# Performance work log

Hardware: AMD Instinct MI355X
Metric: run time of the kernel (lower is better)

The kernel has to match this reference:

```python
import jax, jax.numpy as jnp
import numpy as np

N_NODES = 50000
N_EDGES = 800000
D_IN = 64
D_OUT = 64


def setup_inputs() -> dict:
    key = jax.random.key(0)
    k1, k2, k3, k4 = jax.random.split(key, 4)
    x = jax.random.normal(k1, (N_NODES, D_IN), dtype=jnp.float32)
    src = jax.random.randint(k2, (N_EDGES,), 0, N_NODES, dtype=jnp.int64)
    dst = jax.random.randint(k3, (N_EDGES,), 0, N_NODES, dtype=jnp.int64)
    W = jax.random.normal(k4, (D_IN, D_OUT), dtype=jnp.float32) / np.sqrt(D_IN)
    b = jnp.zeros((D_OUT,), dtype=jnp.float32)
    return {"x": x, "src": src, "dst": dst, "W": W, "b": b}


def reference(x, src, dst, W, b):
    # DGL GraphConv, norm='both': out = D_in^{-1/2} A D_out^{-1/2} x W + b
    n = x.shape[0]
    ones = jnp.ones(src.shape[0], dtype=x.dtype)
    out_deg = jax.ops.segment_sum(ones, src, num_segments=n)  # out-degree of each node
    in_deg = jax.ops.segment_sum(ones, dst, num_segments=n)   # in-degree of each node
    norm_src = jax.lax.rsqrt(jnp.clip(out_deg, 1.0))          # [N]
    norm_dst = jax.lax.rsqrt(jnp.clip(in_deg, 1.0))           # [N]
    h = x * norm_src[:, None]                                 # [N, D_in]
    msg = jnp.take(h, src, axis=0)                            # [E, D_in] gather
    agg = jax.ops.segment_sum(msg, dst, num_segments=n)       # [N, D_in] scatter-add
    agg = agg * norm_dst[:, None]
    return agg @ W + b                                        # [N, D_out]
```

## Files before the change

kernel.cpp:

```cpp
#include <hip/hip_runtime.h>

#define N_NODES 50000
#define N_EDGES 800000
#define D 64

#define SLICES 64
#define I4_PER_SLICE (N_EDGES / 4 / SLICES)
#define NWORDS 12512

#define CTR_OFF    0
#define BASE_OFF   64
#define CUR_OFF    200064
#define SNORM_OFF  400064
#define DNORM_OFF  600064
#define SSRC_OFF   800064
#define PART_OFF   4000064
#define ZERO_BYTES 64

__global__ __launch_bounds__(256) void degree_lds_kernel(const int4* __restrict__ src4,
                                                         const int4* __restrict__ dst4,
                                                         unsigned int* __restrict__ partial) {
    __shared__ unsigned int hist[NWORDS];
    int tid = threadIdx.x;
    for (int i = tid; i < NWORDS; i += 256) hist[i] = 0;
    __syncthreads();

    int role  = blockIdx.x & 1;
    int slice = blockIdx.x >> 1;
    const int4* e = role ? dst4 : src4;
    int beg = slice * I4_PER_SLICE, end = beg + I4_PER_SLICE;
    for (int i = beg + tid; i < end; i += 256) {
        int4 v = e[i];
        atomicAdd(&hist[v.x >> 2], 1u << ((v.x & 3) * 8));
        atomicAdd(&hist[v.y >> 2], 1u << ((v.y & 3) * 8));
        atomicAdd(&hist[v.z >> 2], 1u << ((v.z & 3) * 8));
        atomicAdd(&hist[v.w >> 2], 1u << ((v.w & 3) * 8));
    }
    __syncthreads();

    unsigned int* p = partial + (size_t)blockIdx.x * NWORDS;
    for (int i = tid; i < NWORDS; i += 256) p[i] = hist[i];
}

__global__ __launch_bounds__(256) void merge_scan_kernel(const unsigned int* __restrict__ partial,
                                                         int* __restrict__ base,
                                                         int* __restrict__ cursor,
                                                         float* __restrict__ snorm,
                                                         float* __restrict__ dnorm,
                                                         int* __restrict__ ctr) {
    int n = blockIdx.x * blockDim.x + threadIdx.x;
    int lane = threadIdx.x & 63;
    int din = 0, dout = 0;
    if (n < N_NODES) {
        int w = n >> 2, sh = (n & 3) * 8;
        const unsigned int* po = partial + w;
#pragma unroll 8
        for (int s = 0; s < SLICES; s++) {
            dout += (po[(size_t)(2 * s) * NWORDS] >> sh) & 0xFFu;
            din  += (po[(size_t)(2 * s + 1) * NWORDS] >> sh) & 0xFFu;
        }
    }
    int sum = din;
#pragma unroll
    for (int off = 1; off < 64; off <<= 1) {
        int v = __shfl_up(sum, off);
        if (lane >= off) sum += v;
    }
    int wtot = __shfl(sum, 63);
    int wbase = 0;
    if (lane == 63) wbase = atomicAdd(ctr, wtot);
    wbase = __shfl(wbase, 63);
    if (n < N_NODES) {
        int myb = wbase + (sum - din);
        base[n] = myb;
        cursor[n] = myb;
        dnorm[n] = rsqrtf(fmaxf((float)din, 1.0f));
        snorm[n] = rsqrtf(fmaxf((float)dout, 1.0f));
    }
}

__global__ __launch_bounds__(256) void fill_kernel(const int4* __restrict__ src4,
                                                   const int4* __restrict__ dst4,
                                                   int* __restrict__ cursor,
                                                   int* __restrict__ ssrc) {
    int i = blockIdx.x * blockDim.x + threadIdx.x;
    if (i < N_EDGES / 4) {
        int4 s = src4[i], t = dst4[i];
        int p0 = atomicAdd(&cursor[t.x], 1);
        int p1 = atomicAdd(&cursor[t.y], 1);
        int p2 = atomicAdd(&cursor[t.z], 1);
        int p3 = atomicAdd(&cursor[t.w], 1);
        ssrc[p0] = s.x; ssrc[p1] = s.y; ssrc[p2] = s.z; ssrc[p3] = s.w;
    }
}

#define GBLK 1024
__global__ __launch_bounds__(256, 4) void gather_mm_kernel(const float* __restrict__ x,
                                                           const int* __restrict__ ssrc,
                                                           const int* __restrict__ base,
                                                           const int* __restrict__ cursor,
                                                           const float* __restrict__ snorm,
                                                           const float* __restrict__ dnorm,
                                                           const float* __restrict__ W,
                                                           const float* __restrict__ b,
                                                           float* __restrict__ out) {
    int lane = threadIdx.x & 63;
    int wave = (blockIdx.x << 2) | (threadIdx.x >> 6);

    float Wreg[D];
#pragma unroll
    for (int k = 0; k < D; k++) Wreg[k] = W[k * D + lane];
    float breg = b[lane];
    const float* xl = x + lane;

    for (int n = wave; n < N_NODES; n += GBLK * 4) {
        int beg = base[n];
        int end = cursor[n];
        float a0 = 0.f, a1 = 0.f, a2 = 0.f, a3 = 0.f;
        float a4 = 0.f, a5 = 0.f, a6 = 0.f, a7 = 0.f;
        int i = beg;
        for (; i + 8 <= end; i += 8) {
            int s0 = ssrc[i],     s1 = ssrc[i + 1], s2 = ssrc[i + 2], s3 = ssrc[i + 3];
            int s4 = ssrc[i + 4], s5 = ssrc[i + 5], s6 = ssrc[i + 6], s7 = ssrc[i + 7];
            a0 = fmaf(xl[s0 * D], snorm[s0], a0);
            a1 = fmaf(xl[s1 * D], snorm[s1], a1);
            a2 = fmaf(xl[s2 * D], snorm[s2], a2);
            a3 = fmaf(xl[s3 * D], snorm[s3], a3);
            a4 = fmaf(xl[s4 * D], snorm[s4], a4);
            a5 = fmaf(xl[s5 * D], snorm[s5], a5);
            a6 = fmaf(xl[s6 * D], snorm[s6], a6);
            a7 = fmaf(xl[s7 * D], snorm[s7], a7);
        }
        for (; i + 4 <= end; i += 4) {
            int s0 = ssrc[i], s1 = ssrc[i + 1], s2 = ssrc[i + 2], s3 = ssrc[i + 3];
            a0 = fmaf(xl[s0 * D], snorm[s0], a0);
            a1 = fmaf(xl[s1 * D], snorm[s1], a1);
            a2 = fmaf(xl[s2 * D], snorm[s2], a2);
            a3 = fmaf(xl[s3 * D], snorm[s3], a3);
        }
        for (; i < end; ++i) {
            int s = ssrc[i];
            a0 = fmaf(xl[s * D], snorm[s], a0);
        }
        float acc = ((a0 + a4) + (a1 + a5)) + ((a2 + a6) + (a3 + a7));

        int accb = __float_as_int(acc);
        float p0 = 0.f, p1 = 0.f, p2 = 0.f, p3 = 0.f;
#pragma unroll
        for (int k = 0; k < D; k += 4) {
            p0 = fmaf(__int_as_float(__builtin_amdgcn_readlane(accb, k + 0)), Wreg[k + 0], p0);
            p1 = fmaf(__int_as_float(__builtin_amdgcn_readlane(accb, k + 1)), Wreg[k + 1], p1);
            p2 = fmaf(__int_as_float(__builtin_amdgcn_readlane(accb, k + 2)), Wreg[k + 2], p2);
            p3 = fmaf(__int_as_float(__builtin_amdgcn_readlane(accb, k + 3)), Wreg[k + 3], p3);
        }
        float sum = (p0 + p1) + (p2 + p3);
        out[(size_t)n * D + lane] = fmaf(sum, dnorm[n], breg);
    }
}

extern "C" void kernel_launch(void* const* d_in, const int* in_sizes, int n_in,
                              void* d_out, int out_size, void* d_ws, size_t ws_size,
                              hipStream_t stream) {
    const float* x   = (const float*)d_in[0];
    const int*   src = (const int*)d_in[1];
    const int*   dst = (const int*)d_in[2];
    const float* W   = (const float*)d_in[3];
    const float* b   = (const float*)d_in[4];
    float* out = (float*)d_out;

    char* ws = (char*)d_ws;
    int*          ctr    = (int*)(ws + CTR_OFF);
    int*          base   = (int*)(ws + BASE_OFF);
    int*          cur    = (int*)(ws + CUR_OFF);
    float*        snorm  = (float*)(ws + SNORM_OFF);
    float*        dnorm  = (float*)(ws + DNORM_OFF);
    int*          ssrc   = (int*)(ws + SSRC_OFF);
    unsigned int* part   = (unsigned int*)(ws + PART_OFF);

    hipMemsetAsync(d_ws, 0, ZERO_BYTES, stream);

    {
        degree_lds_kernel<<<2 * SLICES, 256, 0, stream>>>((const int4*)src,
                                                          (const int4*)dst, part);
    }
    {
        int blocks = (N_NODES + 255) / 256;
        merge_scan_kernel<<<blocks, 256, 0, stream>>>(part, base, cur, snorm, dnorm, ctr);
    }
    {
        int blocks = (N_EDGES / 4 + 255) / 256;
        fill_kernel<<<blocks, 256, 0, stream>>>((const int4*)src, (const int4*)dst,
                                                cur, ssrc);
    }
    {
        gather_mm_kernel<<<GBLK, 256, 0, stream>>>(x, ssrc, base, cur,
                                                   snorm, dnorm, W, b, out);
    }
}
```

Baseline: 186.4 us.

## Apply W before gathering, store fp16 projections, and replace atomic fill with slice prefixes

Reassociates the computation so the 64x64 projection is applied once per node (y = (x*snorm) W), and the edge gather sums the precomputed rows. Those rows are stored in fp16, which halves gather traffic at some cost in accuracy. The fill step drops global atomic cursors: a merge pass turns the per-slice LDS histograms into exclusive per-slice prefixes, so each of 80 slice blocks places its edges using LDS atomics alone. This adds two extra kernel launches and leaves the fill running on only 80 blocks.

```diff
diff --git a/kernel.cpp b/kernel.cpp
--- a/kernel.cpp
+++ b/kernel.cpp
@@ -1,20 +1,24 @@
 #include <hip/hip_runtime.h>
+#include <hip/hip_fp16.h>
 
 #define N_NODES 50000
 #define N_EDGES 800000
 #define D 64
 
-#define SLICES 64
-#define I4_PER_SLICE (N_EDGES / 4 / SLICES)
+#define SLICES 80
+#define I4S (N_EDGES / 4 / SLICES)
 #define NWORDS 12512
 
 #define CTR_OFF    0
 #define BASE_OFF   64
-#define CUR_OFF    200064
+#define END_OFF    200064
 #define SNORM_OFF  400064
 #define DNORM_OFF  600064
-#define SSRC_OFF   800064
-#define PART_OFF   4000064
+#define INW_OFF    800064
+#define OUTW_OFF   850112
+#define SSRC_OFF   900160
+#define PART_OFF   4100160
+#define Y16_OFF    PART_OFF
 #define ZERO_BYTES 64
 
 __global__ __launch_bounds__(256) void degree_lds_kernel(const int4* __restrict__ src4,
@@ -28,7 +32,7 @@
     int role  = blockIdx.x & 1;
     int slice = blockIdx.x >> 1;
     const int4* e = role ? dst4 : src4;
-    int beg = slice * I4_PER_SLICE, end = beg + I4_PER_SLICE;
+    int beg = slice * I4S, end = beg + I4S;
     for (int i = beg + tid; i < end; i += 256) {
         int4 v = e[i];
         atomicAdd(&hist[v.x >> 2], 1u << ((v.x & 3) * 8));
@@ -42,23 +46,39 @@
     for (int i = tid; i < NWORDS; i += 256) p[i] = hist[i];
 }
 
-__global__ __launch_bounds__(256) void merge_scan_kernel(const unsigned int* __restrict__ partial,
-                                                         int* __restrict__ base,
-                                                         int* __restrict__ cursor,
-                                                         float* __restrict__ snorm,
-                                                         float* __restrict__ dnorm,
-                                                         int* __restrict__ ctr) {
+__global__ __launch_bounds__(256) void merge_kernel(unsigned int* __restrict__ partial,
+                                                    unsigned int* __restrict__ INW,
+                                                    unsigned int* __restrict__ OUTW) {
+    int w = blockIdx.x * blockDim.x + threadIdx.x;
+    if (w >= 12500) return;
+    unsigned int accin = 0, accout = 0;
+#pragma unroll 4
+    for (int s = 0; s < SLICES; s++) {
+        size_t od = (size_t)(2 * s) * NWORDS + w;
+        size_t dd = (size_t)(2 * s + 1) * NWORDS + w;
+        accout += partial[od];
+        unsigned int v = partial[dd];
+        partial[dd] = accin;
+        accin += v;
+    }
+    INW[w] = accin;
+    OUTW[w] = accout;
+}
+
+__global__ __launch_bounds__(256) void scan_kernel(const unsigned int* __restrict__ INW,
+                                                   const unsigned int* __restrict__ OUTW,
+                                                   int* __restrict__ base,
+                                                   int* __restrict__ rend,
+                                                   float* __restrict__ snorm,
+                                                   float* __restrict__ dnorm,
+                                                   int* __restrict__ ctr) {
     int n = blockIdx.x * blockDim.x + threadIdx.x;
     int lane = threadIdx.x & 63;
     int din = 0, dout = 0;
     if (n < N_NODES) {
-        int w = n >> 2, sh = (n & 3) * 8;
-        const unsigned int* po = partial + w;
-#pragma unroll 8
-        for (int s = 0; s < SLICES; s++) {
-            dout += (po[(size_t)(2 * s) * NWORDS] >> sh) & 0xFFu;
-            din  += (po[(size_t)(2 * s + 1) * NWORDS] >> sh) & 0xFFu;
-        }
+        int sh = (n & 3) * 8;
+        din  = (INW[n >> 2] >> sh) & 0xFF;
+        dout = (OUTW[n >> 2] >> sh) & 0xFF;
     }
     int sum = din;
 #pragma unroll
@@ -73,7 +93,7 @@
     if (n < N_NODES) {
         int myb = wbase + (sum - din);
         base[n] = myb;
-        cursor[n] = myb;
+        rend[n] = myb + din;
         dnorm[n] = rsqrtf(fmaxf((float)din, 1.0f));
         snorm[n] = rsqrtf(fmaxf((float)dout, 1.0f));
     }
@@ -81,80 +101,107 @@
 
 __global__ __launch_bounds__(256) void fill_kernel(const int4* __restrict__ src4,
                                                    const int4* __restrict__ dst4,
-                                                   int* __restrict__ cursor,
+                                                   const unsigned int* __restrict__ partial,
+                                                   const int* __restrict__ base,
                                                    int* __restrict__ ssrc) {
-    int i = blockIdx.x * blockDim.x + threadIdx.x;
-    if (i < N_EDGES / 4) {
-        int4 s = src4[i], t = dst4[i];
-        int p0 = atomicAdd(&cursor[t.x], 1);
-        int p1 = atomicAdd(&cursor[t.y], 1);
-        int p2 = atomicAdd(&cursor[t.z], 1);
-        int p3 = atomicAdd(&cursor[t.w], 1);
-        ssrc[p0] = s.x; ssrc[p1] = s.y; ssrc[p2] = s.z; ssrc[p3] = s.w;
-    }
-}
-
-#define GBLK 1024
-__global__ __launch_bounds__(256, 4) void gather_mm_kernel(const float* __restrict__ x,
-                                                           const int* __restrict__ ssrc,
-                                                           const int* __restrict__ base,
-                                                           const int* __restrict__ cursor,
-                                                           const float* __restrict__ snorm,
-                                                           const float* __restrict__ dnorm,
-                                                           const float* __restrict__ W,
-                                                           const float* __restrict__ b,
-                                                           float* __restrict__ out) {
+    __shared__ unsigned int hist[NWORDS];
+    int tid = threadIdx.x;
+    for (int i = tid; i < NWORDS; i += 256) hist[i] = 0;
+    __syncthreads();
+
+    int s = blockIdx.x;
+    const int4* sp = src4 + (size_t)s * I4S;
+    const int4* dp = dst4 + (size_t)s * I4S;
+    const unsigned int* pref = partial + (size_t)(2 * s + 1) * NWORDS;
+
+    for (int i = tid; i < I4S; i += 256) {
+        int4 sv = sp[i], tv = dp[i];
+#define FILL_ONE(T, S)                                                        \
+        {                                                                     \
+            int t = (T); int sh = (t & 3) * 8;                                \
+            unsigned int old = atomicAdd(&hist[t >> 2], 1u << sh);            \
+            int local = (old >> sh) & 0xFF;                                   \
+            int p = base[t] + (int)((pref[t >> 2] >> sh) & 0xFFu) + local;    \
+            ssrc[p] = (S);                                                    \
+        }
+        FILL_ONE(tv.x, sv.x)
+        FILL_ONE(tv.y, sv.y)
+        FILL_ONE(tv.z, sv.z)
+        FILL_ONE(tv.w, sv.w)
+#undef FILL_ONE
+    }
+}
+
+#define YBLK 1024
+__global__ __launch_bounds__(256, 4) void y_kernel(const float* __restrict__ x,
+                                                   const float* __restrict__ snorm,
+                                                   const float* __restrict__ W,
+                                                   __half* __restrict__ y16) {
     int lane = threadIdx.x & 63;
     int wave = (blockIdx.x << 2) | (threadIdx.x >> 6);
 
     float Wreg[D];
 #pragma unroll
     for (int k = 0; k < D; k++) Wreg[k] = W[k * D + lane];
+
+    for (int n = wave; n < N_NODES; n += YBLK * 4) {
+        float hv = x[(size_t)n * D + lane] * snorm[n];
+        int hb = __float_as_int(hv);
+        float p0 = 0.f, p1 = 0.f, p2 = 0.f, p3 = 0.f;
+#pragma unroll
+        for (int k = 0; k < D; k += 4) {
+            p0 = fmaf(__int_as_float(__builtin_amdgcn_readlane(hb, k + 0)), Wreg[k + 0], p0);
+            p1 = fmaf(__int_as_float(__builtin_amdgcn_readlane(hb, k + 1)), Wreg[k + 1], p1);
+            p2 = fmaf(__int_as_float(__builtin_amdgcn_readlane(hb, k + 2)), Wreg[k + 2], p2);
+            p3 = fmaf(__int_as_float(__builtin_amdgcn_readlane(hb, k + 3)), Wreg[k + 3], p3);
+        }
+        y16[(size_t)n * D + lane] = __float2half((p0 + p1) + (p2 + p3));
+    }
+}
+
+#define GBLK 2048
+__global__ __launch_bounds__(256, 8) void gather_kernel(const __half* __restrict__ y16,
+                                                        const int* __restrict__ ssrc,
+                                                        const int* __restrict__ base,
+                                                        const int* __restrict__ rend,
+                                                        const float* __restrict__ dnorm,
+                                                        const float* __restrict__ b,
+                                                        float* __restrict__ out) {
+    int lane = threadIdx.x & 63;
+    int wave = (blockIdx.x << 2) | (threadIdx.x >> 6);
     float breg = b[lane];
-    const float* xl = x + lane;
+    const __half* yl = y16 + lane;
 
     for (int n = wave; n < N_NODES; n += GBLK * 4) {
         int beg = base[n];
-        int end = cursor[n];
+        int end = rend[n];
         float a0 = 0.f, a1 = 0.f, a2 = 0.f, a3 = 0.f;
         float a4 = 0.f, a5 = 0.f, a6 = 0.f, a7 = 0.f;
         int i = beg;
         for (; i + 8 <= end; i += 8) {
             int s0 = ssrc[i],     s1 = ssrc[i + 1], s2 = ssrc[i + 2], s3 = ssrc[i + 3];
             int s4 = ssrc[i + 4], s5 = ssrc[i + 5], s6 = ssrc[i + 6], s7 = ssrc[i + 7];
-            a0 = fmaf(xl[s0 * D], snorm[s0], a0);
-            a1 = fmaf(xl[s1 * D], snorm[s1], a1);
-            a2 = fmaf(xl[s2 * D], snorm[s2], a2);
-            a3 = fmaf(xl[s3 * D], snorm[s3], a3);
-            a4 = fmaf(xl[s4 * D], snorm[s4], a4);
-            a5 = fmaf(xl[s5 * D], snorm[s5], a5);
-            a6 = fmaf(xl[s6 * D], snorm[s6], a6);
-            a7 = fmaf(xl[s7 * D], snorm[s7], a7);
+            a0 += __half2float(yl[(size_t)s0 * D]);
+            a1 += __half2float(yl[(size_t)s1 * D]);
+            a2 += __half2float(yl[(size_t)s2 * D]);
+            a3 += __half2float(yl[(size_t)s3 * D]);
+            a4 += __half2float(yl[(size_t)s4 * D]);
+            a5 += __half2float(yl[(size_t)s5 * D]);
+            a6 += __half2float(yl[(size_t)s6 * D]);
+            a7 += __half2float(yl[(size_t)s7 * D]);
         }
         for (; i + 4 <= end; i += 4) {
             int s0 = ssrc[i], s1 = ssrc[i + 1], s2 = ssrc[i + 2], s3 = ssrc[i + 3];
-            a0 = fmaf(xl[s0 * D], snorm[s0], a0);
-            a1 = fmaf(xl[s1 * D], snorm[s1], a1);
-            a2 = fmaf(xl[s2 * D], snorm[s2], a2);
-            a3 = fmaf(xl[s3 * D], snorm[s3], a3);
+            a0 += __half2float(yl[(size_t)s0 * D]);
+            a1 += __half2float(yl[(size_t)s1 * D]);
+            a2 += __half2float(yl[(size_t)s2 * D]);
+            a3 += __half2float(yl[(size_t)s3 * D]);
         }
         for (; i < end; ++i) {
-            int s = ssrc[i];
-            a0 = fmaf(xl[s * D], snorm[s], a0);
+            a0 += __half2float(yl[(size_t)ssrc[i] * D]);
         }
         float acc = ((a0 + a4) + (a1 + a5)) + ((a2 + a6) + (a3 + a7));
-
-        int accb = __float_as_int(acc);
-        float p0 = 0.f, p1 = 0.f, p2 = 0.f, p3 = 0.f;
-#pragma unroll
-        for (int k = 0; k < D; k += 4) {
-            p0 = fmaf(__int_as_float(__builtin_amdgcn_readlane(accb, k + 0)), Wreg[k + 0], p0);
-            p1 = fmaf(__int_as_float(__builtin_amdgcn_readlane(accb, k + 1)), Wreg[k + 1], p1);
-            p2 = fmaf(__int_as_float(__builtin_amdgcn_readlane(accb, k + 2)), Wreg[k + 2], p2);
-            p3 = fmaf(__int_as_float(__builtin_amdgcn_readlane(accb, k + 3)), Wreg[k + 3], p3);
-        }
-        float sum = (p0 + p1) + (p2 + p3);
-        out[(size_t)n * D + lane] = fmaf(sum, dnorm[n], breg);
+        out[(size_t)n * D + lane] = fmaf(acc, dnorm[n], breg);
     }
 }
 
@@ -169,31 +216,26 @@
     float* out = (float*)d_out;
 
     char* ws = (char*)d_ws;
-    int*          ctr    = (int*)(ws + CTR_OFF);
-    int*          base   = (int*)(ws + BASE_OFF);
-    int*          cur    = (int*)(ws + CUR_OFF);
-    float*        snorm  = (float*)(ws + SNORM_OFF);
-    float*        dnorm  = (float*)(ws + DNORM_OFF);
-    int*          ssrc   = (int*)(ws + SSRC_OFF);
-    unsigned int* part   = (unsigned int*)(ws + PART_OFF);
+    int*          ctr   = (int*)(ws + CTR_OFF);
+    int*          base  = (int*)(ws + BASE_OFF);
+    int*          rend  = (int*)(ws + END_OFF);
+    float*        snorm = (float*)(ws + SNORM_OFF);
+    float*        dnorm = (float*)(ws + DNORM_OFF);
+    unsigned int* INW   = (unsigned int*)(ws + INW_OFF);
+    unsigned int* OUTW  = (unsigned int*)(ws + OUTW_OFF);
+    int*          ssrc  = (int*)(ws + SSRC_OFF);
+    unsigned int* part  = (unsigned int*)(ws + PART_OFF);
+    __half*       y16   = (__half*)(ws + Y16_OFF);
 
     hipMemsetAsync(d_ws, 0, ZERO_BYTES, stream);
 
-    {
-        degree_lds_kernel<<<2 * SLICES, 256, 0, stream>>>((const int4*)src,
-                                                          (const int4*)dst, part);
-    }
-    {
-        int blocks = (N_NODES + 255) / 256;
-        merge_scan_kernel<<<blocks, 256, 0, stream>>>(part, base, cur, snorm, dnorm, ctr);
-    }
-    {
-        int blocks = (N_EDGES / 4 + 255) / 256;
-        fill_kernel<<<blocks, 256, 0, stream>>>((const int4*)src, (const int4*)dst,
-                                                cur, ssrc);
-    }
-    {
-        gather_mm_kernel<<<GBLK, 256, 0, stream>>>(x, ssrc, base, cur,
-                                                   snorm, dnorm, W, b, out);
-    }
-}
+    degree_lds_kernel<<<2 * SLICES, 256, 0, stream>>>((const int4*)src,
+                                                      (const int4*)dst, part);
+    merge_kernel<<<(12500 + 255) / 256, 256, 0, stream>>>(part, INW, OUTW);
+    scan_kernel<<<(N_NODES + 255) / 256, 256, 0, stream>>>(INW, OUTW, base, rend,
+                                                           snorm, dnorm, ctr);
+    fill_kernel<<<SLICES, 256, 0, stream>>>((const int4*)src, (const int4*)dst,
+                                            part, base, ssrc);
+    y_kernel<<<YBLK, 256, 0, stream>>>(x, snorm, W, y16);
+    gather_kernel<<<GBLK, 256, 0, stream>>>(y16, ssrc, base, rend, dnorm, b, out);
+}
```

After: 171.7 us. 1.09x faster.
